# Kernel tuning notes

Measured on AMD Instinct MI355X. Metric: run time of the kernel, lower is better.

The kernel has to match this reference:

```python
import jax, jax.numpy as jnp
import numpy as np


def _per_patch_bce(logits, labels):
    # numerically stable BCE-with-logits, mean over (C,H,W) -> per-patch loss
    bce = jnp.maximum(logits, 0.0) - logits * labels + jnp.log1p(jnp.exp(-jnp.abs(logits)))
    return bce.mean(axis=(-3, -2, -1))


def setup_inputs() -> dict:
    key = jax.random.key(0)
    k1, k2 = jax.random.split(key)
    B, C, N, M = 64, 1, 128, 136
    inputs = jax.random.normal(k1, (B, C, N, N), dtype=jnp.float32)   # logits
    targets = jax.random.uniform(k2, (B, C, M, M), dtype=jnp.float32)  # soft labels in [0,1]
    return {"inputs": inputs, "targets": targets}


def reference(inputs, targets):
    B, C, N1, N2 = inputs.shape
    M1, M2 = targets.shape[-2], targets.shape[-1]
    s1 = M1 - N1 + 1
    s2 = M2 - N2 + 1
    S = s1 * s2
    center_flat = (s1 // 2) * s2 + (s2 // 2)

    # all (i,j) shift offsets, row-major to match i*shift2+j flattening
    ii, jj = jnp.meshgrid(jnp.arange(s1), jnp.arange(s2), indexing="ij")
    shifts = jnp.stack([ii.ravel(), jj.ravel()], axis=-1)  # (S, 2)

    def extract(ij):
        return jax.lax.dynamic_slice(targets, (0, 0, ij[0], ij[1]), (B, C, N1, N2))

    windows = jax.vmap(extract)(shifts)            # (S, B, C, N, N)
    err = _per_patch_bce(inputs[None], windows)    # (S, B)
    err = err.T                                    # (B, S)

    min_loss = err.min(axis=1)                     # (B,)
    min_ij = err.argmin(axis=1)                    # (B,) first-min tiebreak, as torch.min
    # prefer the center shift when it ties the minimum
    center_is_min = err[:, center_flat] == min_loss
    min_ij = jnp.where(center_is_min, center_flat, min_ij)

    total_loss = min_loss.sum()
    adjusted_labels = windows[min_ij, jnp.arange(B)]  # (B, C, N, N)
    row_shifts = min_ij // s2
    col_shifts = min_ij % s2
    return total_loss, adjusted_labels, (row_shifts, col_shifts)
```

## Files before the change

### kernel.cpp

```cpp
#include <hip/hip_runtime.h>
#include <math.h>

#define B 64
#define N 128
#define M 136
#define S2 9
#define S 81
#define NPIX (N*N)
#define MPIX (M*M)
#define CENTER 40
#define STRIPS 16
#define SROWS 8
#define YR 16
#define YF4S 544

__device__ __forceinline__ float softplus_f(float x) {
    float t = __expf(-fabsf(x));
    return fmaxf(x, 0.0f) + __logf(1.0f + t);
}

#define ROR_ADD(x, CTRL) ((x) + __int_as_float(__builtin_amdgcn_update_dpp( \
        0, __float_as_int(x), (CTRL), 0xf, 0xf, true)))

__global__ __launch_bounds__(256, 4) void k_corr(const float* __restrict__ x,
                                                 const float* __restrict__ y,
                                                 float* __restrict__ D2,
                                                 float* __restrict__ P2) {
    const int tid = threadIdx.x;
    const int b  = blockIdx.x >> 4;
    const int st = blockIdx.x & 15;

    __shared__ float ylds[YR * M];
    __shared__ float part[16][81];
    __shared__ float spart[4];

    const int lr = tid >> 5;
    const int cq = tid & 31;

    const float4 xv = ((const float4*)(x + (size_t)b * NPIX
                                         + (st * SROWS + lr) * N))[cq];

    {
        const float4* ysrc = (const float4*)(y + (size_t)b * MPIX + st * SROWS * M);
        float4* ydst = (float4*)ylds;
        #pragma unroll
        for (int t = 0; t < 3; ++t) {
            int idx = tid + 256 * t;
            if (idx < YF4S) ydst[idx] = ysrc[idx];
        }
    }

    float sp = softplus_f(xv.x) + softplus_f(xv.y)
             + softplus_f(xv.z) + softplus_f(xv.w);

    __syncthreads();

    const int g = tid >> 4;
    const bool lead = (tid & 15) == 0;

    #pragma unroll
    for (int ii = 0; ii < 9; ++ii) {
        const float* yrow = ylds + (lr + ii) * M + cq * 4;
        float4 A  = *(const float4*)(yrow);
        float4 Bq = *(const float4*)(yrow + 4);
        float4 Cq = *(const float4*)(yrow + 8);
        float ya[12];
        ya[0] = A.x;  ya[1] = A.y;  ya[2] = A.z;  ya[3] = A.w;
        ya[4] = Bq.x; ya[5] = Bq.y; ya[6] = Bq.z; ya[7] = Bq.w;
        ya[8] = Cq.x; ya[9] = Cq.y; ya[10] = Cq.z; ya[11] = Cq.w;
        #pragma unroll
        for (int j = 0; j < 9; ++j) {
            float v = xv.x * ya[j]     + xv.y * ya[j + 1]
                    + xv.z * ya[j + 2] + xv.w * ya[j + 3];
            v = ROR_ADD(v, 0x128);
            v = ROR_ADD(v, 0x124);
            v = ROR_ADD(v, 0x122);
            v = ROR_ADD(v, 0x121);
            if (lead) part[g][ii * 9 + j] = v;
        }
    }

    #pragma unroll
    for (int m = 1; m < 64; m <<= 1) sp += __shfl_xor(sp, m, 64);
    if ((tid & 63) == 0) spart[tid >> 6] = sp;
    __syncthreads();

    if (tid < S) {
        float s0 = 0.0f;
        #pragma unroll
        for (int gg = 0; gg < 16; ++gg) s0 += part[gg][tid];
        D2[((size_t)b * STRIPS + st) * S + tid] = s0;
    }
    if (tid == 96) {
        P2[b * STRIPS + st] = (spart[0] + spart[1]) + (spart[2] + spart[3]);
    }
}

__global__ __launch_bounds__(256) void k_out(const float* __restrict__ y,
                                             const float* __restrict__ D2,
                                             const float* __restrict__ P2,
                                             float* __restrict__ out) {
    const int tid = threadIdx.x;
    const int b = blockIdx.x >> 4;
    const int p = blockIdx.x & 15;

    __shared__ float dsum[S];
    __shared__ int sij;

    if (tid < S) {
        float s0 = 0.0f;
        #pragma unroll
        for (int st = 0; st < STRIPS; ++st)
            s0 += D2[((size_t)b * STRIPS + st) * S + tid];
        dsum[tid] = s0;
    }
    __syncthreads();

    if (tid < 64) {
        float bv = dsum[tid];
        int   bi = tid;
        if (tid < S - 64) {
            float v2 = dsum[64 + tid];
            if (v2 > bv) { bv = v2; bi = 64 + tid; }
        }
        #pragma unroll
        for (int m = 1; m < 64; m <<= 1) {
            float ov = __shfl_xor(bv, m, 64);
            int   oi = __shfl_xor(bi, m, 64);
            if (ov > bv || (ov == bv && oi < bi)) { bv = ov; bi = oi; }
        }
        if (tid == 0) {
            if (dsum[CENTER] == bv) bi = CENTER;
            sij = bi;
            if (p == 0) {
                out[1 + B * NPIX + b]     = (float)(bi / S2);
                out[1 + B * NPIX + B + b] = (float)(bi % S2);
                float P = 0.0f;
                #pragma unroll
                for (int st = 0; st < STRIPS; ++st) P += P2[b * STRIPS + st];
                atomicAdd(out, (P - bv) * (1.0f / (float)NPIX));
            }
        }
    }
    __syncthreads();

    {
        const int ij = sij;
        const int i2 = ij / S2, j2 = ij - i2 * S2;
        const int Q = p * 256 + tid;
        const int row = (Q >> 5) + i2;
        const float* yrow = y + (size_t)b * MPIX + row * M + (Q & 31) * 4 + j2;
        float* d = out + 1 + (size_t)b * NPIX + 4 * Q;
        d[0] = yrow[0]; d[1] = yrow[1]; d[2] = yrow[2]; d[3] = yrow[3];
    }
}

extern "C" void kernel_launch(void* const* d_in, const int* in_sizes, int n_in,
                              void* d_out, int out_size, void* d_ws, size_t ws_size,
                              hipStream_t stream) {
    const float* x = (const float*)d_in[0];
    const float* y = (const float*)d_in[1];
    float* out = (float*)d_out;

    float* wsF = (float*)d_ws;
    float* D2  = wsF;
    float* P2  = wsF + B * STRIPS * S;

    k_corr<<<dim3(B * STRIPS), 256, 0, stream>>>(x, y, D2, P2);
    k_out<<<dim3(B * 16), 256, 0, stream>>>(y, D2, P2, out);
}
```

Measured before the change: 74.55 us.

## Fuse correlation and output kernels via last-block-done atomic counter

Merges the two kernels into one. Each strip block bumps a per-batch counter, and the last of the 16 blocks for a batch does the reduction, argmin selection and label copy. The counter lives in the row-shift output slot, which the finishing block later overwrites. This removes a kernel launch and the inter-kernel gap, at the cost of the 16K-pixel copy now running in one block per batch instead of 16. The counter also relies on the output being zero at launch, and it is never reset between calls.

```diff
diff --git a/kernel.cpp b/kernel.cpp
--- a/kernel.cpp
+++ b/kernel.cpp
@@ -22,17 +22,21 @@
 #define ROR_ADD(x, CTRL) ((x) + __int_as_float(__builtin_amdgcn_update_dpp( \
         0, __float_as_int(x), (CTRL), 0xf, 0xf, true)))
 
-__global__ __launch_bounds__(256, 4) void k_corr(const float* __restrict__ x,
-                                                 const float* __restrict__ y,
-                                                 float* __restrict__ D2,
-                                                 float* __restrict__ P2) {
+__global__ __launch_bounds__(256, 4) void k_fused(const float* __restrict__ x,
+                                                  const float* __restrict__ y,
+                                                  float* __restrict__ D2,
+                                                  float* __restrict__ P2,
+                                                  float* __restrict__ out) {
     const int tid = threadIdx.x;
-    const int b  = blockIdx.x >> 4;
-    const int st = blockIdx.x & 15;
+    const int b  = blockIdx.x & 63;
+    const int st = blockIdx.x >> 6;
 
     __shared__ float ylds[YR * M];
     __shared__ float part[16][81];
     __shared__ float spart[4];
+    __shared__ float dsum[S];
+    __shared__ int sflag;
+    __shared__ int sij;
 
     const int lr = tid >> 5;
     const int cq = tid & 31;
@@ -94,24 +98,22 @@
     if (tid == 96) {
         P2[b * STRIPS + st] = (spart[0] + spart[1]) + (spart[2] + spart[3]);
     }
-}
 
-__global__ __launch_bounds__(256) void k_out(const float* __restrict__ y,
-                                             const float* __restrict__ D2,
-                                             const float* __restrict__ P2,
-                                             float* __restrict__ out) {
-    const int tid = threadIdx.x;
-    const int b = blockIdx.x >> 4;
-    const int p = blockIdx.x & 15;
-
-    __shared__ float dsum[S];
-    __shared__ int sij;
+    __syncthreads();
+    if (tid == 0) {
+        __threadfence();
+        float old = atomicAdd(&out[1 + B * NPIX + b], 1.0f);
+        sflag = (old >= 15.0f) ? 1 : 0;
+    }
+    __syncthreads();
+    if (sflag == 0) return;
+    __threadfence();
 
     if (tid < S) {
         float s0 = 0.0f;
         #pragma unroll
-        for (int st = 0; st < STRIPS; ++st)
-            s0 += D2[((size_t)b * STRIPS + st) * S + tid];
+        for (int ss = 0; ss < STRIPS; ++ss)
+            s0 += D2[((size_t)b * STRIPS + ss) * S + tid];
         dsum[tid] = s0;
     }
     __syncthreads();
@@ -132,14 +134,12 @@
         if (tid == 0) {
             if (dsum[CENTER] == bv) bi = CENTER;
             sij = bi;
-            if (p == 0) {
-                out[1 + B * NPIX + b]     = (float)(bi / S2);
-                out[1 + B * NPIX + B + b] = (float)(bi % S2);
-                float P = 0.0f;
-                #pragma unroll
-                for (int st = 0; st < STRIPS; ++st) P += P2[b * STRIPS + st];
-                atomicAdd(out, (P - bv) * (1.0f / (float)NPIX));
-            }
+            out[1 + B * NPIX + b]     = (float)(bi / S2);
+            out[1 + B * NPIX + B + b] = (float)(bi % S2);
+            float P = 0.0f;
+            #pragma unroll
+            for (int ss = 0; ss < STRIPS; ++ss) P += P2[b * STRIPS + ss];
+            atomicAdd(out, (P - bv) * (1.0f / (float)NPIX));
         }
     }
     __syncthreads();
@@ -147,11 +147,16 @@
     {
         const int ij = sij;
         const int i2 = ij / S2, j2 = ij - i2 * S2;
-        const int Q = p * 256 + tid;
-        const int row = (Q >> 5) + i2;
-        const float* yrow = y + (size_t)b * MPIX + row * M + (Q & 31) * 4 + j2;
-        float* d = out + 1 + (size_t)b * NPIX + 4 * Q;
-        d[0] = yrow[0]; d[1] = yrow[1]; d[2] = yrow[2]; d[3] = yrow[3];
+        const float* yb = y + (size_t)b * MPIX;
+        float* dstB = out + 1 + (size_t)b * NPIX;
+        #pragma unroll
+        for (int k2 = 0; k2 < 16; ++k2) {
+            const int Q = tid + 256 * k2;
+            const int row = (Q >> 5) + i2;
+            const float* yrow = yb + row * M + (Q & 31) * 4 + j2;
+            float* d = dstB + 4 * Q;
+            d[0] = yrow[0]; d[1] = yrow[1]; d[2] = yrow[2]; d[3] = yrow[3];
+        }
     }
 }
 
@@ -166,6 +171,5 @@
     float* D2  = wsF;
     float* P2  = wsF + B * STRIPS * S;
 
-    k_corr<<<dim3(B * STRIPS), 256, 0, stream>>>(x, y, D2, P2);
-    k_out<<<dim3(B * 16), 256, 0, stream>>>(y, D2, P2, out);
+    k_fused<<<dim3(B * STRIPS), 256, 0, stream>>>(x, y, D2, P2, out);
 }
```

Result: slower. 92.38 us (+23.9%).
